# Kernel tuning notes

Measured on AMD Instinct MI355X. Metric: run time of the kernel, lower is better.

The kernel has to match this reference:

```python
import jax, jax.numpy as jnp
import numpy as np

V, E, H, HC = 20000, 300, 512, 256
B, N, LE, NW, LW, NC, LC = 16, 64, 16, 8, 16, 64, 16


def _gru_dir(xg, W_hh, b_hh, reverse):
    # xg: [B, T, 3*Hc] precomputed input gates; returns final hidden [B, Hc]
    xs = jnp.swapaxes(xg, 0, 1)
    if reverse:
        xs = xs[::-1]
    h0 = jnp.zeros((xg.shape[0], W_hh.shape[1]), xg.dtype)

    def step(h, xt):
        hr, hz, hn = jnp.split(h @ W_hh.T + b_hh, 3, axis=-1)
        xr, xz, xn = jnp.split(xt, 3, axis=-1)
        r = jax.nn.sigmoid(xr + hr)
        z = jax.nn.sigmoid(xz + hz)
        n = jnp.tanh(xn + r * hn)
        return (1.0 - z) * n + z * h, None

    hT, _ = jax.lax.scan(step, h0, xs)
    return hT


def _bigru(x, Wif, Whf, bif, bhf, Wib, Whb, bib, bhb):
    # x: [B, T, D] -> concat(fwd final, bwd final) = [B, 2*Hc]  (matches torch h_n.permute(1,0,2).reshape)
    hf = _gru_dir(x @ Wif.T + bif, Whf, bhf, False)
    hb = _gru_dir(x @ Wib.T + bib, Whb, bhb, True)
    return jnp.concatenate([hf, hb], axis=-1)


def setup_inputs() -> dict:
    key = jax.random.key(0)
    ks = iter(jax.random.split(key, 64))
    f = lambda *s: jax.random.normal(next(ks), s, jnp.float32) * 0.05
    ri = lambda *s: jax.random.randint(next(ks), s, 0, V)
    return {
        "emb_table": f(V, E),
        "W_prj": f(H, E),
        "dn_Wif": f(3 * HC, H), "dn_Whf": f(3 * HC, HC), "dn_bif": f(3 * HC), "dn_bhf": f(3 * HC),
        "dn_Wib": f(3 * HC, H), "dn_Whb": f(3 * HC, HC), "dn_bib": f(3 * HC), "dn_bhb": f(3 * HC),
        "W_e": f(H, H), "W_l": f(H, H), "W_w": f(H, H),
        "Wg": f(H, H), "bg": f(H),
        "diff_Wif": f(3 * H, H), "diff_Whf": f(3 * H, H), "diff_bif": f(3 * H), "diff_bhf": f(3 * H),
        "diff_Wib": f(3 * H, H), "diff_Whb": f(3 * H, H), "diff_bib": f(3 * H), "diff_bhb": f(3 * H),
        "Wc": f(1, 2 * H), "bc": f(1),
        "Wa1": f(2 * H, 2 * H), "ba1": f(2 * H), "Wa2": f(1, 2 * H), "ba2": f(1),
        "local_adj": jnp.zeros((64, 64), jnp.float32),
        "obs": ri(B, 32),
        "local_graph": ri(64, 8),
        "entities": ri(B, N, LE),
        "locals_": ri(B, N, LE),
        "worlds": ri(B, N, NW, LW),
        "commands": ri(B, NC, LC),
    }


def reference(emb_table, W_prj,
              dn_Wif, dn_Whf, dn_bif, dn_bhf, dn_Wib, dn_Whb, dn_bib, dn_bhb,
              W_e, W_l, W_w, Wg, bg,
              diff_Wif, diff_Whf, diff_bif, diff_bhf, diff_Wib, diff_Whb, diff_bib, diff_bhb,
              Wc, bc, Wa1, ba1, Wa2, ba2,
              local_adj, obs, local_graph, entities, locals_, worlds, commands):
    dn = (dn_Wif, dn_Whf, dn_bif, dn_bhf, dn_Wib, dn_Whb, dn_bib, dn_bhb)
    emb = lambda ids: emb_table[ids] @ W_prj.T  # embedding lookup + no-bias projection to H

    b, n, le = entities.shape
    ent_h = _bigru(emb(entities).reshape(b * n, le, H), *dn).reshape(b, n, H)
    ll = locals_.shape[-1]
    loc_h = _bigru(emb(locals_).reshape(b * n, ll, H), *dn).reshape(b, n, H)
    nw, lw = worlds.shape[2], worlds.shape[3]
    w_h = _bigru(emb(worlds).reshape(b * n * nw, lw, H), *dn).reshape(b, n, nw, H)
    worlds_sum = (w_h @ W_w).sum(axis=2)  # [b, n, H]

    # torch.ones(H,H) + W_e  ==  broadcastable 1.0 + W_e
    graph_hidden = jax.nn.elu(ent_h @ (1.0 + W_e)) + jax.nn.elu(loc_h @ W_l) + worlds_sum
    graph_encoding = jax.nn.elu(jax.nn.elu(graph_hidden) @ Wg.T + bg)  # graph_prj (dropout=eval identity)

    # value network: 'diff' path
    diff_h = _bigru(graph_encoding, diff_Wif, diff_Whf, diff_bif, diff_bhf,
                    diff_Wib, diff_Whb, diff_bib, diff_bhb)  # [b, 2H]
    value = (diff_h @ Wc.T + bc).reshape(b, 1, 1)

    nc, lc = commands.shape[1], commands.shape[2]
    c_h = _bigru(emb(commands).reshape(b * nc, lc, H), *dn).reshape(b, nc, H)

    rep = jnp.concatenate([
        jnp.broadcast_to(c_h[:, None, :, :], (b, n, nc, H)),
        jnp.broadcast_to(graph_encoding[:, :, None, :], (b, n, nc, H)),
    ], axis=-1)  # [b, n, nc, 2H]
    s = jax.nn.elu(rep @ Wa1.T + ba1) @ Wa2.T + ba2  # att_cmd (dropout p=0)
    scores = s[..., 0].mean(axis=1)  # mean over entities -> [b, nc]

    mask = commands.sum(axis=2) > 0
    probs = jax.nn.softmax(jnp.where(mask, scores, -1e9), axis=1)
    index = jnp.argmax(probs, axis=1).reshape(1, b, 1)  # deterministic stand-in for multinomial(1)
    return scores, index, value
```

## Files before the change

### kernel.cpp

```cpp
#include <hip/hip_runtime.h>
#include <stdint.h>

#define DEVFN __device__ __forceinline__

typedef __attribute__((ext_vector_type(4))) float fx4;
typedef __attribute__((ext_vector_type(8))) short sx8;
typedef __bf16 bf16x8 __attribute__((ext_vector_type(8)));

DEVFN float eluf(float x){ return x>0.f ? x : __expf(x)-1.f; }
DEVFN float sigm(float x){ return 1.f/(1.f+__expf(-x)); }
DEVFN float tanhf_(float x){ float cx=fminf(10.f,fmaxf(-10.f,x)); float e=__expf(-2.f*cx); return (1.f-e)/(1.f+e); }

DEVFN fx4 MFMA(sx8 a, sx8 b, fx4 c){
  return __builtin_amdgcn_mfma_f32_16x16x32_bf16(
      __builtin_bit_cast(bf16x8,a), __builtin_bit_cast(bf16x8,b), c, 0,0,0);
}
DEVFN void splitf(float x, short& hi, short& lo){
  __bf16 h = (__bf16)x; hi = __builtin_bit_cast(short, h);
  __bf16 l = (__bf16)(x - (float)h); lo = __builtin_bit_cast(short, l);
}

struct TT { const float* src; float* dst; int srows, scols, drows; };
struct TTs { TT t[4]; };
__global__ void k_prep_t(TTs ts){
  TT tk = ts.t[blockIdx.y];
  size_t tot = (size_t)tk.drows * tk.srows;
  for (size_t i = (size_t)blockIdx.x*256 + threadIdx.x; i < tot; i += (size_t)gridDim.x*256){
    int c = (int)(i / tk.srows), r = (int)(i % tk.srows);
    tk.dst[i] = (c < tk.scols) ? tk.src[(size_t)r*tk.scols + c] : 0.f;
  }
}
struct PL { const float* src; __bf16* hi; __bf16* lo; size_t n; };
struct PLs { PL t[2]; };
__global__ void k_prep_planes(PLs ts){
  PL tk = ts.t[blockIdx.y];
  for (size_t i = (size_t)blockIdx.x*256 + threadIdx.x; i < tk.n; i += (size_t)gridDim.x*256){
    float x = tk.src[i];
    __bf16 h = (__bf16)x;
    tk.hi[i] = h; tk.lo[i] = (__bf16)(x - (float)h);
  }
}
struct BC { const float* src; __bf16* dst; size_t n; };
struct BCs { BC t[2]; };
__global__ void k_prep_b16(BCs ts){
  BC tk = ts.t[blockIdx.y];
  for (size_t i = (size_t)blockIdx.x*256 + threadIdx.x; i < tk.n; i += (size_t)gridDim.x*256)
    tk.dst[i] = (__bf16)tk.src[i];
}
__global__ void k_toks(const int* __restrict__ ents, const int* __restrict__ locs,
                       const int* __restrict__ wrl, const int* __restrict__ cmd,
                       int* __restrict__ toks){
  int idx = blockIdx.x*256 + threadIdx.x;
  if (idx >= 2*16*11264) return;
  int dir = idx / (16*11264);
  int rem = idx % (16*11264);
  int s = rem / 11264, c = rem % 11264;
  const int* tp;
  if (c<1024) tp = ents + c*16;
  else if (c<2048) tp = locs + (c-1024)*16;
  else if (c<10240) tp = wrl + (c-2048)*16;
  else tp = cmd + (c-10240)*16;
  toks[idx] = tp[dir ? 15-s : s];
}
__global__ void k_cat_bias(const float* __restrict__ a, const float* __restrict__ b,
                           float* __restrict__ o){
  int i = blockIdx.x*256 + threadIdx.x;
  if (i < 768) o[i] = a[i];
  else if (i < 1536) o[i] = b[i-768];
}

template<int EPI, int OBF>
__global__ __launch_bounds__(256) void gemm_k(
    const float* __restrict__ A, const float* __restrict__ B,
    const float* __restrict__ bias, void* __restrict__ out,
    int M, int N, int Kpad, int Kreal, int lda, int ldb)
{
  int bm = blockIdx.y*64, bn = blockIdx.x*64;
  int tid = threadIdx.x, l = tid&63, w = tid>>6;
  int wm = (w>>1)*32, wn = (w&1)*32;
  int lr = l&15, lk = l>>4;
  fx4 acc[2][2] = {};
  for (int k0 = 0; k0 < Kpad; k0 += 32) {
    sx8 ahi[2], alo[2], bhi[2], blo[2];
    bool full = (k0 + 32 <= Kreal);
    #pragma unroll
    for (int i=0;i<2;i++){
      int row = bm + wm + i*16 + lr; row = row < M ? row : M-1;
      int col = bn + wn + i*16 + lr;
      const float* ap = A + (size_t)row*lda + k0 + lk*8;
      const float* bp = B + (size_t)col*ldb + k0 + lk*8;
      float av[8], bv[8];
      if (full){
        *(fx4*)av = *(const fx4*)ap; *(fx4*)(av+4) = *(const fx4*)(ap+4);
        *(fx4*)bv = *(const fx4*)bp; *(fx4*)(bv+4) = *(const fx4*)(bp+4);
      } else {
        #pragma unroll
        for (int j=0;j<8;j++){
          int k = k0 + lk*8 + j;
          av[j] = (k < Kreal) ? ap[j] : 0.f;
          bv[j] = (k < Kreal) ? bp[j] : 0.f;
        }
      }
      #pragma unroll
      for (int j=0;j<8;j++){
        short h,lo2; splitf(av[j], h, lo2); ahi[i][j]=h; alo[i][j]=lo2;
        splitf(bv[j], h, lo2); bhi[i][j]=h; blo[i][j]=lo2;
      }
    }
    #pragma unroll
    for (int i=0;i<2;i++)
      #pragma unroll
      for (int j=0;j<2;j++){
        acc[i][j] = MFMA(alo[i], bhi[j], acc[i][j]);
        acc[i][j] = MFMA(ahi[i], blo[j], acc[i][j]);
        acc[i][j] = MFMA(ahi[i], bhi[j], acc[i][j]);
      }
  }
  #pragma unroll
  for (int i=0;i<2;i++)
    #pragma unroll
    for (int j=0;j<2;j++)
      #pragma unroll
      for (int q=0;q<4;q++){
        int m = bm + wm + i*16 + lk*4 + q;
        int n = bn + wn + j*16 + lr;
        if (m < M){
          float v = acc[i][j][q];
          if (EPI>=1) v += bias[n];
          if (EPI==2) v = eluf(v);
          if (OBF) ((__bf16*)out)[(size_t)m*N + n] = (__bf16)v;
          else     ((float*)out)[(size_t)m*N + n] = v;
        }
      }
}

__global__ __launch_bounds__(256) void dn_step(
  const __bf16* __restrict__ Hshi, const __bf16* __restrict__ Hslo,
  __bf16* __restrict__ Hdhi, __bf16* __restrict__ Hdlo,
  const __bf16* __restrict__ Whi, const __bf16* __restrict__ Wlo,
  const float* __restrict__ bias, const float* __restrict__ T, int tstride,
  const int* __restrict__ toks,
  float* __restrict__ seqh, int s, int dir)
{
  int bm = blockIdx.x*64;
  int bj = blockIdx.y*64;
  int tid = threadIdx.x, l = tid&63, w = tid>>6;
  int wm = (w>>1)*32, wn = (w&1)*32;
  int lr = l&15, lk = l>>4;
  const int* tks = toks + s*11264;
  float xv[2][4][2][3];
  #pragma unroll
  for (int i=0;i<2;i++){
    #pragma unroll
    for (int q=0;q<4;q++){
      int m = bm + wm + i*16 + lk*4 + q;
      const float* trow = T + (size_t)tks[m]*tstride;
      #pragma unroll
      for (int jt=0;jt<2;jt++){
        int j = bj + wn + jt*16 + lr;
        xv[i][q][jt][0] = trow[j];
        xv[i][q][jt][1] = trow[256+j];
        xv[i][q][jt][2] = trow[512+j];
      }
    }
  }
  fx4 acc[2][2][3] = {};
  if (s > 0){
    for (int kk=0;kk<8;kk++){
      sx8 ah[2], al[2];
      #pragma unroll
      for (int i=0;i<2;i++){
        int m = bm + wm + i*16 + lr;
        ah[i] = *(const sx8*)(Hshi + (size_t)m*256 + kk*32 + lk*8);
        al[i] = *(const sx8*)(Hslo + (size_t)m*256 + kk*32 + lk*8);
      }
      #pragma unroll
      for (int jt=0;jt<2;jt++){
        #pragma unroll
        for (int role=0;role<3;role++){
          int col = role*256 + bj + wn + jt*16 + lr;
          sx8 bhf = *(const sx8*)(Whi + (size_t)col*256 + kk*32 + lk*8);
          sx8 blf = *(const sx8*)(Wlo + (size_t)col*256 + kk*32 + lk*8);
          #pragma unroll
          for (int i=0;i<2;i++){
            fx4 a = acc[i][jt][role];
            a = MFMA(al[i], bhf, a);
            a = MFMA(ah[i], blf, a);
            a = MFMA(ah[i], bhf, a);
            acc[i][jt][role] = a;
          }
        }
      }
    }
  }
  #pragma unroll
  for (int i=0;i<2;i++){
    #pragma unroll
    for (int q=0;q<4;q++){
      int m = bm + wm + i*16 + lk*4 + q;
      #pragma unroll
      for (int jt=0;jt<2;jt++){
        int j = bj + wn + jt*16 + lr;
        float hr = acc[i][jt][0][q] + bias[j];
        float hz = acc[i][jt][1][q] + bias[256+j];
        float hn = acc[i][jt][2][q] + bias[512+j];
        float xr = xv[i][q][jt][0], xz = xv[i][q][jt][1], xn = xv[i][q][jt][2];
        float ho = 0.f;
        if (s > 0) ho = (float)Hshi[(size_t)m*256+j] + (float)Hslo[(size_t)m*256+j];
        float r = sigm(xr+hr), z = sigm(xz+hz);
        float n = tanhf_(xn + r*hn);
        float v = (1.f-z)*n + z*ho;
        __bf16 hh = (__bf16)v;
        Hdhi[(size_t)m*256+j] = hh;
        Hdlo[(size_t)m*256+j] = (__bf16)(v - (float)hh);
        if (s == 15) seqh[(size_t)m*512 + dir*256 + j] = v;
      }
    }
  }
}

__global__ void k_wsum(const float* __restrict__ seqh, float* __restrict__ ws){
  int r = blockIdx.x;
  for (int c = threadIdx.x; c < 512; c += 256){
    float a = 0.f;
    #pragma unroll
    for (int w8=0; w8<8; w8++) a += seqh[((size_t)2048 + r*8 + w8)*512 + c];
    ws[(size_t)r*512 + c] = a;
  }
}
__global__ void k_rowsum(const float* __restrict__ seqh, float* __restrict__ rs){
  int r = blockIdx.x, l = threadIdx.x;
  float a = 0.f;
  for (int c=l;c<512;c+=64) a += seqh[(size_t)r*512+c];
  #pragma unroll
  for (int o=32;o>0;o>>=1) a += __shfl_down(a,o);
  if (l==0) rs[r]=a;
}
__global__ void k_combine(const float* __restrict__ E1, const float* __restrict__ E2,
                          const float* __restrict__ E3, const float* __restrict__ rs,
                          float* __restrict__ y){
  size_t i = (size_t)blockIdx.x*256 + threadIdx.x;
  int r = (int)(i >> 9);
  float g = eluf(E1[i] + rs[r]) + eluf(E2[i]) + E3[i];
  y[i] = eluf(g);
}

__global__ __launch_bounds__(256) void diff_step(
  const float* __restrict__ hsrc, float* __restrict__ hdst,
  const __bf16* __restrict__ Whf, const __bf16* __restrict__ Whb,
  const float* __restrict__ bhf, const float* __restrict__ bhb,
  const __bf16* __restrict__ Xf, const __bf16* __restrict__ Xb, int t)
{
  int wg = blockIdx.x;
  int dir = wg>>3, seg = wg&7;
  const __bf16* W = dir? Whb: Whf;
  const float* bh = dir? bhb: bhf;
  const __bf16* X = dir? Xb: Xf;
  int tt = dir? 63-t : t;
  int tid = threadIdx.x, l = tid&63, w = tid>>6;
  int lr=l&15, lk=l>>4;
  int jbase = seg*64 + w*16;
  fx4 acc[3] = {};
  const float* hrow = hsrc + (size_t)dir*16*512;
  for (int kk=0;kk<16;kk++){
    const float* ap = hrow + (size_t)lr*512 + kk*32 + lk*8;
    float av[8];
    *(fx4*)av = *(const fx4*)ap; *(fx4*)(av+4) = *(const fx4*)(ap+4);
    sx8 ah, al;
    #pragma unroll
    for (int j=0;j<8;j++){ short h,lo; splitf(av[j],h,lo); ah[j]=h; al[j]=lo; }
    #pragma unroll
    for (int role=0;role<3;role++){
      int col = role*512 + jbase + lr;
      sx8 b = *(const sx8*)(W + (size_t)col*512 + kk*32 + lk*8);
      acc[role] = MFMA(al, b, acc[role]);
      acc[role] = MFMA(ah, b, acc[role]);
    }
  }
  #pragma unroll
  for (int q=0;q<4;q++){
    int m = lk*4+q;
    int j = jbase + lr;
    float hr = acc[0][q] + bh[j];
    float hz = acc[1][q] + bh[512+j];
    float hn = acc[2][q] + bh[1024+j];
    const __bf16* xrow = X + ((size_t)m*64 + tt)*1536;
    float xr = (float)xrow[j], xz = (float)xrow[512+j], xn = (float)xrow[1024+j];
    float ho = hrow[(size_t)m*512 + j];
    float r = sigm(xr+hr), z = sigm(xz+hz);
    float n = tanhf_(xn + r*hn);
    hdst[((size_t)dir*16 + m)*512 + j] = (1.f-z)*n + z*ho;
  }
}

__global__ __launch_bounds__(256) void k_score(
  const float* __restrict__ Amat, const float* __restrict__ Gmat,
  const float* __restrict__ Wa2, const float* __restrict__ ba2, float* __restrict__ sc)
{
  __shared__ float red[4];
  int p = blockIdx.x, b = p>>6, tid = threadIdx.x;
  float av[4], wv[4];
  #pragma unroll
  for (int k=0;k<4;k++){ av[k] = Amat[(size_t)p*1024 + tid + k*256]; wv[k] = Wa2[tid + k*256]; }
  float acc = 0.f;
  for (int n=0;n<64;n++){
    const float* g = Gmat + ((size_t)b*64+n)*1024;
    #pragma unroll
    for (int k=0;k<4;k++) acc += wv[k]*eluf(av[k] + g[tid + k*256]);
  }
  #pragma unroll
  for (int o=32;o>0;o>>=1) acc += __shfl_down(acc,o);
  if ((tid&63)==0) red[tid>>6] = acc;
  __syncthreads();
  if (tid==0) sc[p] = (red[0]+red[1]+red[2]+red[3])*(1.f/64.f) + ba2[0];
}

__global__ void k_final(const float* __restrict__ sc, const int* __restrict__ cmds,
                        const float* __restrict__ hfin, const float* __restrict__ Wc,
                        const float* __restrict__ bc, float* __restrict__ out)
{
  int b = blockIdx.x, l = threadIdx.x;
  out[b*64+l] = sc[b*64+l];
  int ssum = 0;
  const int* cr = cmds + (b*64+l)*16;
  #pragma unroll
  for (int k=0;k<16;k++) ssum += cr[k];
  float v = ssum>0 ? sc[b*64+l] : -1e9f;
  int idx = l;
  #pragma unroll
  for (int o=32;o>0;o>>=1){
    float ov = __shfl_down(v,o); int oi = __shfl_down(idx,o);
    if (ov > v || (ov==v && oi<idx)) { v=ov; idx=oi; }
  }
  if (l==0) out[1024 + b] = (float)idx;
  float a = 0.f;
  for (int j=l;j<512;j+=64) a += hfin[(size_t)b*512+j] * Wc[j];
  for (int j=l;j<512;j+=64) a += hfin[(size_t)(16+b)*512+j] * Wc[512+j];
  #pragma unroll
  for (int o=32;o>0;o>>=1) a += __shfl_down(a,o);
  if (l==0) out[1040 + b] = a + bc[0];
}

static inline void launch_gemm(hipStream_t st, const float* A, const float* B,
                               const float* bias, void* out, int M, int N,
                               int Kpad, int Kreal, int lda, int ldb, int epi, int obf)
{
  dim3 g(N/64, (M+63)/64), blk(256);
  if      (epi==0 && obf==0) gemm_k<0,0><<<g,blk,0,st>>>(A,B,bias,out,M,N,Kpad,Kreal,lda,ldb);
  else if (epi==1 && obf==0) gemm_k<1,0><<<g,blk,0,st>>>(A,B,bias,out,M,N,Kpad,Kreal,lda,ldb);
  else if (epi==2 && obf==0) gemm_k<2,0><<<g,blk,0,st>>>(A,B,bias,out,M,N,Kpad,Kreal,lda,ldb);
  else                       gemm_k<1,1><<<g,blk,0,st>>>(A,B,bias,out,M,N,Kpad,Kreal,lda,ldb);
}

extern "C" void kernel_launch(void* const* d_in, const int* in_sizes, int n_in,
                              void* d_out, int out_size, void* d_ws, size_t ws_size,
                              hipStream_t stream) {
  (void)in_sizes; (void)n_in; (void)out_size;
  const float* emb   = (const float*)d_in[0];
  const float* W_prj = (const float*)d_in[1];
  const float* dnWif = (const float*)d_in[2];
  const float* dnWhf = (const float*)d_in[3];
  const float* dnbif = (const float*)d_in[4];
  const float* dnbhf = (const float*)d_in[5];
  const float* dnWib = (const float*)d_in[6];
  const float* dnWhb = (const float*)d_in[7];
  const float* dnbib = (const float*)d_in[8];
  const float* dnbhb = (const float*)d_in[9];
  const float* W_e   = (const float*)d_in[10];
  const float* W_l   = (const float*)d_in[11];
  const float* W_w   = (const float*)d_in[12];
  const float* Wg    = (const float*)d_in[13];
  const float* bg    = (const float*)d_in[14];
  const float* dWif  = (const float*)d_in[15];
  const float* dWhf  = (const float*)d_in[16];
  const float* dbif  = (const float*)d_in[17];
  const float* dbhf  = (const float*)d_in[18];
  const float* dWib  = (const float*)d_in[19];
  const float* dWhb  = (const float*)d_in[20];
  const float* dbib  = (const float*)d_in[21];
  const float* dbhb  = (const float*)d_in[22];
  const float* Wc    = (const float*)d_in[23];
  const float* bc    = (const float*)d_in[24];
  const float* Wa1   = (const float*)d_in[25];
  const float* ba1   = (const float*)d_in[26];
  const float* Wa2   = (const float*)d_in[27];
  const float* ba2   = (const float*)d_in[28];
  const int* ents = (const int*)d_in[32];
  const int* locs = (const int*)d_in[33];
  const int* wrl  = (const int*)d_in[34];
  const int* cmds = (const int*)d_in[35];

  char* ws = (char*)d_ws;
  size_t off = 0;
#define WSP(name, type, count) type* name = (type*)(ws + off); off += (((size_t)(count))*sizeof(type) + 255) & ~(size_t)255;
  WSP(pWprjT, float, 320*512);
  WSP(pC2,    float, 1536*320);
  WSP(pB2,    float, 1536);
  WSP(pWhFhi, __bf16, 768*256);
  WSP(pWhFlo, __bf16, 768*256);
  WSP(pWhBhi, __bf16, 768*256);
  WSP(pWhBlo, __bf16, 768*256);
  WSP(pWeT,   float, 512*512);
  WSP(pWlT,   float, 512*512);
  WSP(pWwT,   float, 512*512);
  WSP(pdWhF,  __bf16, 1536*512);
  WSP(pdWhB,  __bf16, 1536*512);
  WSP(pSeqh,  float, 11264*512);
  WSP(pH0hi,  __bf16, 11264*256);
  WSP(pH0lo,  __bf16, 11264*256);
  WSP(pH1hi,  __bf16, 11264*256);
  WSP(pH1lo,  __bf16, 11264*256);
  WSP(pToks,  int,    2*16*11264);
  WSP(pHA,    float, 32*512);
  WSP(pHB,    float, 32*512);
  WSP(pRs,    float, 1024);
  WSP(pScf,   float, 1024);
#undef WSP
  float* pT = (float*)(ws + off);
  size_t trem = (ws_size > off) ? (ws_size - off) : 0;
  const size_t TBL = (size_t)20000*1536*sizeof(float);
  bool comb = trem >= TBL;

  const size_t SZ = (size_t)1024*512*4;
  char* sc = (char*)pT;
  float* pWsum = (float*)(sc + 0*SZ);
  float* pE1   = (float*)(sc + 1*SZ);
  float* pE2   = (float*)(sc + 2*SZ);
  float* pE3   = (float*)(sc + 3*SZ);
  float* pY    = (float*)(sc + 4*SZ);
  float* pGe   = (float*)(sc + 5*SZ);
  float* pAmat = (float*)(sc + 6*SZ);
  float* pGmat = (float*)(sc + 8*SZ);
  __bf16* pXf  = (__bf16*)(sc + 10*SZ);
  __bf16* pXb  = (__bf16*)(sc + 10*SZ + (size_t)1024*1536*2);

  TTs tt;
  tt.t[0] = { W_prj, pWprjT, 512, 300, 320 };
  tt.t[1] = { W_e,   pWeT,   512, 512, 512 };
  tt.t[2] = { W_l,   pWlT,   512, 512, 512 };
  tt.t[3] = { W_w,   pWwT,   512, 512, 512 };
  k_prep_t<<<dim3(256,4), 256, 0, stream>>>(tt);
  PLs pl;
  pl.t[0] = { dnWhf, pWhFhi, pWhFlo, (size_t)768*256 };
  pl.t[1] = { dnWhb, pWhBhi, pWhBlo, (size_t)768*256 };
  k_prep_planes<<<dim3(256,2), 256, 0, stream>>>(pl);
  BCs bcs;
  bcs.t[0] = { dWhf, pdWhF, (size_t)1536*512 };
  bcs.t[1] = { dWhb, pdWhB, (size_t)1536*512 };
  k_prep_b16<<<dim3(512,2), 256, 0, stream>>>(bcs);
  k_toks<<<1408, 256, 0, stream>>>(ents, locs, wrl, cmds, pToks);
  k_cat_bias<<<6, 256, 0, stream>>>(dnbif, dnbib, pB2);

  launch_gemm(stream, dnWif, pWprjT, nullptr, pC2,           768, 320, 512, 512, 512, 512, 0, 0);
  launch_gemm(stream, dnWib, pWprjT, nullptr, pC2 + 768*320, 768, 320, 512, 512, 512, 512, 0, 0);

  if (comb){
    launch_gemm(stream, emb, pC2, pB2, pT, 20000, 1536, 320, 300, 300, 320, 1, 0);
    for (int dir = 0; dir < 2; ++dir){
      const __bf16* Whi = dir? pWhBhi : pWhFhi;
      const __bf16* Wlo = dir? pWhBlo : pWhFlo;
      const float*  bh  = dir? dnbhb  : dnbhf;
      const int*    tks = pToks + (size_t)dir*16*11264;
      const float*  Td  = pT + dir*768;
      for (int s = 0; s < 16; ++s){
        __bf16 *shi, *slo, *dhi, *dlo;
        if ((s & 1) == 0){ shi=pH0hi; slo=pH0lo; dhi=pH1hi; dlo=pH1lo; }
        else             { shi=pH1hi; slo=pH1lo; dhi=pH0hi; dlo=pH0lo; }
        dn_step<<<dim3(176,4), 256, 0, stream>>>(shi, slo, dhi, dlo,
            Whi, Wlo, bh, Td, 1536, tks, pSeqh, s, dir);
      }
    }
  } else {
    for (int dir = 0; dir < 2; ++dir){
      launch_gemm(stream, emb, dir? pC2 + 768*320 : pC2, dir? dnbib : dnbif, pT,
                  20000, 768, 320, 300, 300, 320, 1, 0);
      const __bf16* Whi = dir? pWhBhi : pWhFhi;
      const __bf16* Wlo = dir? pWhBlo : pWhFlo;
      const float*  bh  = dir? dnbhb  : dnbhf;
      const int*    tks = pToks + (size_t)dir*16*11264;
      for (int s = 0; s < 16; ++s){
        __bf16 *shi, *slo, *dhi, *dlo;
        if ((s & 1) == 0){ shi=pH0hi; slo=pH0lo; dhi=pH1hi; dlo=pH1lo; }
        else             { shi=pH1hi; slo=pH1lo; dhi=pH0hi; dlo=pH0lo; }
        dn_step<<<dim3(176,4), 256, 0, stream>>>(shi, slo, dhi, dlo,
            Whi, Wlo, bh, pT, 768, tks, pSeqh, s, dir);
      }
    }
  }

  k_wsum<<<1024, 256, 0, stream>>>(pSeqh, pWsum);
  k_rowsum<<<1024, 64, 0, stream>>>(pSeqh, pRs);
  launch_gemm(stream, pSeqh,                   pWeT, nullptr, pE1, 1024, 512, 512, 512, 512, 512, 0, 0);
  launch_gemm(stream, pSeqh + (size_t)1024*512,pWlT, nullptr, pE2, 1024, 512, 512, 512, 512, 512, 0, 0);
  launch_gemm(stream, pWsum,                   pWwT, nullptr, pE3, 1024, 512, 512, 512, 512, 512, 0, 0);
  k_combine<<<2048, 256, 0, stream>>>(pE1, pE2, pE3, pRs, pY);
  launch_gemm(stream, pY, Wg, bg, pGe, 1024, 512, 512, 512, 512, 512, 2, 0);
  launch_gemm(stream, pGe, dWif, dbif, pXf, 1024, 1536, 512, 512, 512, 512, 1, 1);
  launch_gemm(stream, pGe, dWib, dbib, pXb, 1024, 1536, 512, 512, 512, 512, 1, 1);
  launch_gemm(stream, pSeqh + (size_t)10240*512, Wa1, nullptr, pAmat, 1024, 1024, 512, 512, 512, 1024, 0, 0);
  launch_gemm(stream, pGe, Wa1 + 512, ba1, pGmat, 1024, 1024, 512, 512, 512, 1024, 1, 0);
  k_score<<<1024, 256, 0, stream>>>(pAmat, pGmat, Wa2, ba2, pScf);
  hipMemsetAsync(pHA, 0, 32*512*sizeof(float), stream);
  float* ha = pHA; float* hb = pHB;
  for (int t=0; t<64; ++t){
    diff_step<<<16, 256, 0, stream>>>(ha, hb, pdWhF, pdWhB, dbhf, dbhb, pXf, pXb, t);
    float* tmp = ha; ha = hb; hb = tmp;
  }
  k_final<<<16, 64, 0, stream>>>(pScf, cmds, ha, Wc, bc, (float*)d_out);
}
```

Baseline: 3.154 ms.

## Replace per-step GRU launches with persistent kernel and grid barrier; split-bf16 table GEMM

Merges the 16 per-timestep dn_step launches per direction into one persistent kernel of 704 blocks. The blocks synchronise between timesteps through an atomic counter barrier, and the next step's input-gate rows are prefetched before the barrier. The embedding-table projection GEMM now runs on MFMA using hi/lo bf16 splits of the embedding and projection matrices, prepared by a new split kernel. The persistent kernel depends on all 704 blocks being resident at once, which launch_bounds(256,3) is meant to allow. If they are not all resident it can deadlock, and the split adds extra preprocessing passes over the 20000x320 table.

```diff
diff --git a/kernel.cpp b/kernel.cpp
--- a/kernel.cpp
+++ b/kernel.cpp
@@ -38,6 +38,16 @@
     float x = tk.src[i];
     __bf16 h = (__bf16)x;
     tk.hi[i] = h; tk.lo[i] = (__bf16)(x - (float)h);
+  }
+}
+__global__ void k_split(const float* __restrict__ src, __bf16* __restrict__ hi,
+                        __bf16* __restrict__ lo, int rows, int cin, int cout, int stride){
+  size_t tot = (size_t)rows * cout;
+  for (size_t i = (size_t)blockIdx.x*256 + threadIdx.x; i < tot; i += (size_t)gridDim.x*256){
+    int r = (int)(i / cout), c = (int)(i % cout);
+    float x = (c < cin) ? src[(size_t)r*stride + c] : 0.f;
+    __bf16 h = (__bf16)x;
+    hi[i] = h; lo[i] = (__bf16)(x - (float)h);
   }
 }
 struct BC { const float* src; __bf16* dst; size_t n; };
@@ -134,87 +144,162 @@
       }
 }
 
-__global__ __launch_bounds__(256) void dn_step(
-  const __bf16* __restrict__ Hshi, const __bf16* __restrict__ Hslo,
-  __bf16* __restrict__ Hdhi, __bf16* __restrict__ Hdlo,
+__global__ __launch_bounds__(256) void gemm_tbl(
+    const __bf16* __restrict__ Ahi, const __bf16* __restrict__ Alo,
+    const __bf16* __restrict__ Bhi, const __bf16* __restrict__ Blo,
+    const float* __restrict__ bias, float* __restrict__ out,
+    int M, int N, int K)
+{
+  int bm = blockIdx.y*64, bn = blockIdx.x*64;
+  int tid = threadIdx.x, l = tid&63, w = tid>>6;
+  int wm = (w>>1)*32, wn = (w&1)*32;
+  int lr = l&15, lk = l>>4;
+  fx4 acc[2][2] = {};
+  for (int k0 = 0; k0 < K; k0 += 32) {
+    sx8 ah[2], al[2], bh[2], bl[2];
+    #pragma unroll
+    for (int i=0;i<2;i++){
+      int row = bm + wm + i*16 + lr; row = row < M ? row : M-1;
+      int col = bn + wn + i*16 + lr;
+      ah[i] = *(const sx8*)(Ahi + (size_t)row*K + k0 + lk*8);
+      al[i] = *(const sx8*)(Alo + (size_t)row*K + k0 + lk*8);
+      bh[i] = *(const sx8*)(Bhi + (size_t)col*K + k0 + lk*8);
+      bl[i] = *(const sx8*)(Blo + (size_t)col*K + k0 + lk*8);
+    }
+    #pragma unroll
+    for (int i=0;i<2;i++)
+      #pragma unroll
+      for (int j=0;j<2;j++){
+        acc[i][j] = MFMA(al[i], bh[j], acc[i][j]);
+        acc[i][j] = MFMA(ah[i], bl[j], acc[i][j]);
+        acc[i][j] = MFMA(ah[i], bh[j], acc[i][j]);
+      }
+  }
+  #pragma unroll
+  for (int i=0;i<2;i++)
+    #pragma unroll
+    for (int j=0;j<2;j++)
+      #pragma unroll
+      for (int q=0;q<4;q++){
+        int m = bm + wm + i*16 + lk*4 + q;
+        int n = bn + wn + j*16 + lr;
+        if (m < M) out[(size_t)m*N + n] = acc[i][j][q] + bias[n];
+      }
+}
+
+__global__ __launch_bounds__(256,3) void dn_persist(
+  __bf16* __restrict__ H0hi, __bf16* __restrict__ H0lo,
+  __bf16* __restrict__ H1hi, __bf16* __restrict__ H1lo,
   const __bf16* __restrict__ Whi, const __bf16* __restrict__ Wlo,
   const float* __restrict__ bias, const float* __restrict__ T, int tstride,
   const int* __restrict__ toks,
-  float* __restrict__ seqh, int s, int dir)
-{
-  int bm = blockIdx.x*64;
-  int bj = blockIdx.y*64;
+  float* __restrict__ seqh, int dir, unsigned* __restrict__ bar)
+{
+  int bx = blockIdx.x;
+  int bm = (bx >> 2) * 64;
+  int bj = (bx & 3) * 64;
   int tid = threadIdx.x, l = tid&63, w = tid>>6;
   int wm = (w>>1)*32, wn = (w&1)*32;
   int lr = l&15, lk = l>>4;
-  const int* tks = toks + s*11264;
+
   float xv[2][4][2][3];
-  #pragma unroll
-  for (int i=0;i<2;i++){
-    #pragma unroll
-    for (int q=0;q<4;q++){
-      int m = bm + wm + i*16 + lk*4 + q;
-      const float* trow = T + (size_t)tks[m]*tstride;
-      #pragma unroll
-      for (int jt=0;jt<2;jt++){
-        int j = bj + wn + jt*16 + lr;
-        xv[i][q][jt][0] = trow[j];
-        xv[i][q][jt][1] = trow[256+j];
-        xv[i][q][jt][2] = trow[512+j];
-      }
-    }
-  }
-  fx4 acc[2][2][3] = {};
-  if (s > 0){
-    for (int kk=0;kk<8;kk++){
-      sx8 ah[2], al[2];
-      #pragma unroll
-      for (int i=0;i<2;i++){
-        int m = bm + wm + i*16 + lr;
-        ah[i] = *(const sx8*)(Hshi + (size_t)m*256 + kk*32 + lk*8);
-        al[i] = *(const sx8*)(Hslo + (size_t)m*256 + kk*32 + lk*8);
-      }
-      #pragma unroll
-      for (int jt=0;jt<2;jt++){
+  {
+    const int* tks = toks;
+    #pragma unroll
+    for (int i=0;i<2;i++)
+      #pragma unroll
+      for (int q=0;q<4;q++){
+        int m = bm + wm + i*16 + lk*4 + q;
+        const float* trow = T + (size_t)tks[m]*tstride;
         #pragma unroll
-        for (int role=0;role<3;role++){
-          int col = role*256 + bj + wn + jt*16 + lr;
-          sx8 bhf = *(const sx8*)(Whi + (size_t)col*256 + kk*32 + lk*8);
-          sx8 blf = *(const sx8*)(Wlo + (size_t)col*256 + kk*32 + lk*8);
+        for (int jt=0;jt<2;jt++){
+          int j = bj + wn + jt*16 + lr;
+          xv[i][q][jt][0]=trow[j]; xv[i][q][jt][1]=trow[256+j]; xv[i][q][jt][2]=trow[512+j];
+        }
+      }
+  }
+
+  for (int s=0; s<16; ++s){
+    const __bf16 *Hshi, *Hslo; __bf16 *Hdhi, *Hdlo;
+    if ((s&1)==0){ Hshi=H0hi; Hslo=H0lo; Hdhi=H1hi; Hdlo=H1lo; }
+    else         { Hshi=H1hi; Hslo=H1lo; Hdhi=H0hi; Hdlo=H0lo; }
+
+    fx4 acc[2][2][3] = {};
+    if (s > 0){
+      for (int kk=0;kk<8;kk++){
+        sx8 ah[2], al[2];
+        #pragma unroll
+        for (int i=0;i<2;i++){
+          int m = bm + wm + i*16 + lr;
+          ah[i] = *(const sx8*)(Hshi + (size_t)m*256 + kk*32 + lk*8);
+          al[i] = *(const sx8*)(Hslo + (size_t)m*256 + kk*32 + lk*8);
+        }
+        #pragma unroll
+        for (int jt=0;jt<2;jt++){
           #pragma unroll
-          for (int i=0;i<2;i++){
-            fx4 a = acc[i][jt][role];
-            a = MFMA(al[i], bhf, a);
-            a = MFMA(ah[i], blf, a);
-            a = MFMA(ah[i], bhf, a);
-            acc[i][jt][role] = a;
+          for (int role=0;role<3;role++){
+            int col = role*256 + bj + wn + jt*16 + lr;
+            sx8 bhf = *(const sx8*)(Whi + (size_t)col*256 + kk*32 + lk*8);
+            sx8 blf = *(const sx8*)(Wlo + (size_t)col*256 + kk*32 + lk*8);
+            #pragma unroll
+            for (int i=0;i<2;i++){
+              fx4 a = acc[i][jt][role];
+              a = MFMA(al[i], bhf, a);
+              a = MFMA(ah[i], blf, a);
+              a = MFMA(ah[i], bhf, a);
+              acc[i][jt][role] = a;
+            }
           }
         }
       }
     }
-  }
-  #pragma unroll
-  for (int i=0;i<2;i++){
-    #pragma unroll
-    for (int q=0;q<4;q++){
-      int m = bm + wm + i*16 + lk*4 + q;
-      #pragma unroll
-      for (int jt=0;jt<2;jt++){
-        int j = bj + wn + jt*16 + lr;
-        float hr = acc[i][jt][0][q] + bias[j];
-        float hz = acc[i][jt][1][q] + bias[256+j];
-        float hn = acc[i][jt][2][q] + bias[512+j];
-        float xr = xv[i][q][jt][0], xz = xv[i][q][jt][1], xn = xv[i][q][jt][2];
-        float ho = 0.f;
-        if (s > 0) ho = (float)Hshi[(size_t)m*256+j] + (float)Hslo[(size_t)m*256+j];
-        float r = sigm(xr+hr), z = sigm(xz+hz);
-        float n = tanhf_(xn + r*hn);
-        float v = (1.f-z)*n + z*ho;
-        __bf16 hh = (__bf16)v;
-        Hdhi[(size_t)m*256+j] = hh;
-        Hdlo[(size_t)m*256+j] = (__bf16)(v - (float)hh);
-        if (s == 15) seqh[(size_t)m*512 + dir*256 + j] = v;
-      }
+    #pragma unroll
+    for (int i=0;i<2;i++){
+      #pragma unroll
+      for (int q=0;q<4;q++){
+        int m = bm + wm + i*16 + lk*4 + q;
+        #pragma unroll
+        for (int jt=0;jt<2;jt++){
+          int j = bj + wn + jt*16 + lr;
+          float hr = acc[i][jt][0][q] + bias[j];
+          float hz = acc[i][jt][1][q] + bias[256+j];
+          float hn = acc[i][jt][2][q] + bias[512+j];
+          float ho = 0.f;
+          if (s > 0) ho = (float)Hshi[(size_t)m*256+j] + (float)Hslo[(size_t)m*256+j];
+          float r = sigm(xv[i][q][jt][0]+hr), z = sigm(xv[i][q][jt][1]+hz);
+          float n = tanhf_(xv[i][q][jt][2] + r*hn);
+          float v = (1.f-z)*n + z*ho;
+          __bf16 hh = (__bf16)v;
+          Hdhi[(size_t)m*256+j] = hh;
+          Hdlo[(size_t)m*256+j] = (__bf16)(v - (float)hh);
+          if (s == 15) seqh[(size_t)m*512 + dir*256 + j] = v;
+        }
+      }
+    }
+    if (s < 15){
+      const int* tks = toks + (s+1)*11264;
+      #pragma unroll
+      for (int i=0;i<2;i++)
+        #pragma unroll
+        for (int q=0;q<4;q++){
+          int m = bm + wm + i*16 + lk*4 + q;
+          const float* trow = T + (size_t)tks[m]*tstride;
+          #pragma unroll
+          for (int jt=0;jt<2;jt++){
+            int j = bj + wn + jt*16 + lr;
+            xv[i][q][jt][0]=trow[j]; xv[i][q][jt][1]=trow[256+j]; xv[i][q][jt][2]=trow[512+j];
+          }
+        }
+      __threadfence();
+      __syncthreads();
+      if (tid==0){
+        atomicAdd(bar, 1u);
+        unsigned tgt = 704u*(unsigned)(s+1);
+        while (__hip_atomic_load(bar, __ATOMIC_RELAXED, __HIP_MEMORY_SCOPE_AGENT) < tgt)
+          __builtin_amdgcn_s_sleep(2);
+      }
+      __syncthreads();
+      __threadfence();
     }
   }
 }
@@ -396,6 +481,10 @@
   WSP(pWprjT, float, 320*512);
   WSP(pC2,    float, 1536*320);
   WSP(pB2,    float, 1536);
+  WSP(pEhi,   __bf16, 20000*320);
+  WSP(pElo,   __bf16, 20000*320);
+  WSP(pC2hi,  __bf16, 1536*320);
+  WSP(pC2lo,  __bf16, 1536*320);
   WSP(pWhFhi, __bf16, 768*256);
   WSP(pWhFlo, __bf16, 768*256);
   WSP(pWhBhi, __bf16, 768*256);
@@ -415,6 +504,7 @@
   WSP(pHB,    float, 32*512);
   WSP(pRs,    float, 1024);
   WSP(pScf,   float, 1024);
+  WSP(pBar,   unsigned, 64);
 #undef WSP
   float* pT = (float*)(ws + off);
   size_t trem = (ws_size > off) ? (ws_size - off) : 0;
@@ -450,41 +540,29 @@
   k_prep_b16<<<dim3(512,2), 256, 0, stream>>>(bcs);
   k_toks<<<1408, 256, 0, stream>>>(ents, locs, wrl, cmds, pToks);
   k_cat_bias<<<6, 256, 0, stream>>>(dnbif, dnbib, pB2);
+  k_split<<<2048, 256, 0, stream>>>(emb, pEhi, pElo, 20000, 300, 320, 300);
 
   launch_gemm(stream, dnWif, pWprjT, nullptr, pC2,           768, 320, 512, 512, 512, 512, 0, 0);
   launch_gemm(stream, dnWib, pWprjT, nullptr, pC2 + 768*320, 768, 320, 512, 512, 512, 512, 0, 0);
-
+  k_split<<<512, 256, 0, stream>>>(pC2, pC2hi, pC2lo, 1536, 320, 320, 320);
+
+  hipMemsetAsync(pBar, 0, 64*sizeof(unsigned), stream);
   if (comb){
-    launch_gemm(stream, emb, pC2, pB2, pT, 20000, 1536, 320, 300, 300, 320, 1, 0);
+    gemm_tbl<<<dim3(1536/64, 313), 256, 0, stream>>>(pEhi, pElo, pC2hi, pC2lo,
+        pB2, pT, 20000, 1536, 320);
     for (int dir = 0; dir < 2; ++dir){
-      const __bf16* Whi = dir? pWhBhi : pWhFhi;
-      const __bf16* Wlo = dir? pWhBlo : pWhFlo;
-      const float*  bh  = dir? dnbhb  : dnbhf;
-      const int*    tks = pToks + (size_t)dir*16*11264;
-      const float*  Td  = pT + dir*768;
-      for (int s = 0; s < 16; ++s){
-        __bf16 *shi, *slo, *dhi, *dlo;
-        if ((s & 1) == 0){ shi=pH0hi; slo=pH0lo; dhi=pH1hi; dlo=pH1lo; }
-        else             { shi=pH1hi; slo=pH1lo; dhi=pH0hi; dlo=pH0lo; }
-        dn_step<<<dim3(176,4), 256, 0, stream>>>(shi, slo, dhi, dlo,
-            Whi, Wlo, bh, Td, 1536, tks, pSeqh, s, dir);
-      }
+      dn_persist<<<704, 256, 0, stream>>>(pH0hi, pH0lo, pH1hi, pH1lo,
+          dir? pWhBhi : pWhFhi, dir? pWhBlo : pWhFlo, dir? dnbhb : dnbhf,
+          pT + dir*768, 1536, pToks + (size_t)dir*16*11264, pSeqh, dir, pBar + dir);
     }
   } else {
     for (int dir = 0; dir < 2; ++dir){
-      launch_gemm(stream, emb, dir? pC2 + 768*320 : pC2, dir? dnbib : dnbif, pT,
-                  20000, 768, 320, 300, 300, 320, 1, 0);
-      const __bf16* Whi = dir? pWhBhi : pWhFhi;
-      const __bf16* Wlo = dir? pWhBlo : pWhFlo;
-      const float*  bh  = dir? dnbhb  : dnbhf;
-      const int*    tks = pToks + (size_t)dir*16*11264;
-      for (int s = 0; s < 16; ++s){
-        __bf16 *shi, *slo, *dhi, *dlo;
-        if ((s & 1) == 0){ shi=pH0hi; slo=pH0lo; dhi=pH1hi; dlo=pH1lo; }
-        else             { shi=pH1hi; slo=pH1lo; dhi=pH0hi; dlo=pH0lo; }
-        dn_step<<<dim3(176,4), 256, 0, stream>>>(shi, slo, dhi, dlo,
-            Whi, Wlo, bh, pT, 768, tks, pSeqh, s, dir);
-      }
+      gemm_tbl<<<dim3(768/64, 313), 256, 0, stream>>>(pEhi, pElo,
+          pC2hi + (size_t)dir*768*320, pC2lo + (size_t)dir*768*320,
+          dir? dnbib : dnbif, pT, 20000, 768, 320);
+      dn_persist<<<704, 256, 0, stream>>>(pH0hi, pH0lo, pH1hi, pH1lo,
+          dir? pWhBhi : pWhFhi, dir? pWhBlo : pWhFlo, dir? dnbhb : dnbhf,
+          pT, 768, pToks + (size_t)dir*16*11264, pSeqh, dir, pBar + dir);
     }
   }
 
```

After: 9.795 ms. 211% more time.
